# Optimization experiments

Hardware: AMD Instinct MI355X
Metric: run time of the kernel (lower is better)

Reference implementation:

```python
import jax, jax.numpy as jnp
import numpy as np

B, D, CTX, H = 262144, 16, 128, 192
IN_DIM = D + CTX + 1  # 145


def _linear_init(k, fan_in, fan_out):
    bound = 1.0 / np.sqrt(fan_in)
    kw, kb = jax.random.split(k)
    W = jax.random.uniform(kw, (fan_in, fan_out), jnp.float32, -bound, bound)
    b = jax.random.uniform(kb, (fan_out,), jnp.float32, -bound, bound)
    return W, b


def setup_inputs() -> dict:
    key = jax.random.key(0)
    ks = jax.random.split(key, 7)
    W1, b1 = _linear_init(ks[0], IN_DIM, H)
    W2, b2 = _linear_init(ks[1], H, H)
    W3, b3 = _linear_init(ks[2], H, D)
    return {
        "t": jax.random.uniform(ks[3], (), jnp.float32),
        "y": jax.random.normal(ks[4], (B, D), jnp.float32),
        "logp": jnp.zeros((B,), jnp.float32),
        "h": jax.random.normal(ks[5], (B, CTX), jnp.float32),
        "eps": jax.random.normal(ks[6], (B, D), jnp.float32),
        "W1": W1, "b1": b1, "W2": W2, "b2": b2, "W3": W3, "b3": b3,
    }


def _mlp(x, W1, b1, W2, b2, W3, b3):
    # 3-layer MLP, exact (erf) GELU as torch.nn.GELU default
    x = jax.nn.gelu(x @ W1 + b1, approximate=False)
    x = jax.nn.gelu(x @ W2 + b2, approximate=False)
    return x @ W3 + b3


def reference(t, y, logp, h, eps, W1, b1, W2, b2, W3, b3):
    Bsz = y.shape[0]
    t_feat = jnp.ones((Bsz, 1), y.dtype) * t

    def f_of_y(yy):
        inp = jnp.concatenate([yy, h, t_feat], axis=1)  # (B, D+CTX+1)
        return _mlp(inp, W1, b1, W2, b2, W3, b3)  # (B, D)

    # Hutchinson: torch computes g = J^T eps then (g*eps).sum(1) = eps^T J^T eps,
    # which per-row equals eps^T J eps = dot(eps, J eps). Forward-mode JVP computes
    # f and J eps in one fused pass (same math, no explicit backward graph).
    f, Jeps = jax.jvp(f_of_y, (y,), (eps,))
    trace = jnp.sum(Jeps * eps, axis=1)  # (B,)
    dlogp = -trace
    dh = jnp.zeros_like(h)
    return (f, dlogp, dh)
```

## Files before the change

kernel.cpp:

```cpp
#include <hip/hip_runtime.h>
#include <hip/hip_bf16.h>
#include <math.h>

#define B_TOTAL 262144
#define D 16
#define CTX 128
#define H 192
#define IN_DIM 145
#define KP1 160
#define M 32
#define BLOCK 256

typedef __attribute__((ext_vector_type(8))) short bf16x8;
typedef __attribute__((ext_vector_type(4))) float f32x4;

#define MFMA(a, b, c) __builtin_amdgcn_mfma_f32_16x16x32_bf16((a), (b), (c), 0, 0, 0)

__device__ __forceinline__ unsigned short f2bf_rne(float f) {
    unsigned u = __builtin_bit_cast(unsigned, f);
    u += 0x7FFFu + ((u >> 16) & 1u);
    return (unsigned short)(u >> 16);
}
__device__ __forceinline__ void split2(float v, unsigned short& hi, unsigned short& lo) {
    unsigned u = __builtin_bit_cast(unsigned, v);
    hi = (unsigned short)(u >> 16);
    float hf = __builtin_bit_cast(float, u & 0xFFFF0000u);
    lo = f2bf_rne(v - hf);
}
__device__ __forceinline__ void gelu_pair(float x, float& a, float& gp) {
    float s   = x * x;
    float e   = __expf(-0.5f * s);
    float az  = fabsf(x) * 0.70710678118654752f;
    float t   = __builtin_amdgcn_rcpf(fmaf(0.3275911f, az, 1.0f));
    float p   = t * (0.254829592f + t * (-0.284496736f + t * (1.421413741f +
                t * (-1.453152027f + t * 1.061405429f))));
    float erfv = __builtin_copysignf(1.0f - p * e, x);
    float phi  = fmaf(0.5f, erfv, 0.5f);
    gp = fmaf(0.39894228040143268f * x, e, phi);
    a  = x * phi;
}

__global__ void prep_weights(const float* __restrict__ W1,
                             const float* __restrict__ W2,
                             const float* __restrict__ W3,
                             unsigned short* __restrict__ wt)
{
    int i = blockIdx.x * 256 + threadIdx.x;
    if (i < H * KP1) {
        int n = i / KP1, kp = i % KP1;
        float v = 0.0f;
        if (kp < 16)       v = W1[kp * H + n];
        else if (kp == 16) v = W1[144 * H + n];
        else if (kp >= 32) v = W1[(kp - 16) * H + n];
        wt[i] = f2bf_rne(v);
        return;
    }
    i -= H * KP1;
    if (i < H * H) {
        int n = i / H, k = i % H;
        wt[30720 + i] = f2bf_rne(W2[k * H + n]);
        return;
    }
    i -= H * H;
    if (i < D * H) {
        int n = i / H, k = i % H;
        wt[67584 + i] = f2bf_rne(W3[k * D + n]);
    }
}

__global__ __launch_bounds__(BLOCK, 3) void odefunc_mfma(
    const float* __restrict__ t_ptr,
    const float* __restrict__ y,
    const float* __restrict__ h,
    const float* __restrict__ eps,
    const float* __restrict__ b1,
    const float* __restrict__ b2,
    const float* __restrict__ b3,
    const unsigned short* __restrict__ wt,
    float* __restrict__ out_f,
    float* __restrict__ out_dlogp,
    float* __restrict__ out_dh)
{
    __shared__ __align__(16) unsigned short Xh[M][168];
    __shared__ __align__(16) unsigned short Xl[M][40];
    __shared__ __align__(16) unsigned short Th[M][40], Tl[M][40];
    __shared__ __align__(16) unsigned short A[M][200], U[M][200];

    const int tid  = threadIdx.x;
    const int lane = tid & 63;
    const int wv   = tid >> 6;
    const int quad = lane >> 4;
    const int l16  = lane & 15;
    const size_t r0 = (size_t)blockIdx.x * M;

    const unsigned short* Wt1 = wt;
    const unsigned short* Wt2 = wt + 30720;
    const unsigned short* Wt3 = wt + 67584;

    {
        float4 z4 = {0.f, 0.f, 0.f, 0.f};
        #pragma unroll
        for (int i = 0; i < 4; ++i) {
            int idx = tid + i * BLOCK;
            int r = idx >> 5, c4 = (idx & 31) * 4;
            *(float4*)(out_dh + (r0 + r) * CTX + c4) = z4;
        }
    }

    {
        int task = tid >> 7, idx = tid & 127;
        int r = idx >> 2, d4 = (idx & 3) * 4;
        const float* src = task ? eps : y;
        float4 v = *(const float4*)(src + (r0 + r) * D + d4);
        ushort4 hi, lo;
        split2(v.x, hi.x, lo.x); split2(v.y, hi.y, lo.y);
        split2(v.z, hi.z, lo.z); split2(v.w, hi.w, lo.w);
        if (task == 0) { *(ushort4*)&Xh[r][d4] = hi; *(ushort4*)&Xl[r][d4] = lo; }
        else           { *(ushort4*)&Th[r][d4] = hi; *(ushort4*)&Tl[r][d4] = lo; }
    }
    if (tid < M) {
        int r = tid;
        float tv = t_ptr[0];
        unsigned short thi, tlo;
        split2(tv, thi, tlo);
        ushort4 z4 = {0, 0, 0, 0};
        ushort4 t4 = {thi, 0, 0, 0};
        ushort4 l4 = {tlo, 0, 0, 0};
        *(ushort4*)&Xh[r][16] = t4; *(ushort4*)&Xh[r][20] = z4;
        *(ushort4*)&Xh[r][24] = z4; *(ushort4*)&Xh[r][28] = z4;
        *(ushort4*)&Xl[r][16] = l4; *(ushort4*)&Xl[r][20] = z4;
        *(ushort4*)&Xl[r][24] = z4; *(ushort4*)&Xl[r][28] = z4;
        *(ushort4*)&Th[r][16] = z4; *(ushort4*)&Th[r][20] = z4;
        *(ushort4*)&Th[r][24] = z4; *(ushort4*)&Th[r][28] = z4;
        *(ushort4*)&Tl[r][16] = z4; *(ushort4*)&Tl[r][20] = z4;
        *(ushort4*)&Tl[r][24] = z4; *(ushort4*)&Tl[r][28] = z4;
    }
    #pragma unroll
    for (int i = 0; i < 4; ++i) {
        int idx = tid + i * BLOCK;
        int r = idx >> 5, c4 = (idx & 31) * 4;
        float4 v = *(const float4*)(h + (r0 + r) * CTX + c4);
        ushort4 hv = { f2bf_rne(v.x), f2bf_rne(v.y), f2bf_rne(v.z), f2bf_rne(v.w) };
        *(ushort4*)&Xh[r][32 + c4] = hv;
    }
    __syncthreads();

    const f32x4 zf = {0.f, 0.f, 0.f, 0.f};

    f32x4 z[2][3], u[2][3];
    #pragma unroll
    for (int rt = 0; rt < 2; ++rt)
        #pragma unroll
        for (int j = 0; j < 3; ++j) { z[rt][j] = zf; u[rt][j] = zf; }

    bf16x8 w1f[3][5];
    #pragma unroll
    for (int j = 0; j < 3; ++j) {
        int n = (wv * 3 + j) * 16 + l16;
        #pragma unroll
        for (int kc = 0; kc < 5; ++kc)
            w1f[j][kc] = *(const bf16x8*)(Wt1 + n * KP1 + kc * 32 + quad * 8);
    }
    #pragma unroll
    for (int kc = 0; kc < 5; ++kc)
        #pragma unroll
        for (int rt = 0; rt < 2; ++rt) {
            bf16x8 ah = *(const bf16x8*)&Xh[rt * 16 + l16][kc * 32 + quad * 8];
            #pragma unroll
            for (int j = 0; j < 3; ++j) z[rt][j] = MFMA(ah, w1f[j][kc], z[rt][j]);
        }
    #pragma unroll
    for (int rt = 0; rt < 2; ++rt) {
        int m = rt * 16 + l16;
        bf16x8 al = *(const bf16x8*)&Xl[m][quad * 8];
        bf16x8 th = *(const bf16x8*)&Th[m][quad * 8];
        bf16x8 tl = *(const bf16x8*)&Tl[m][quad * 8];
        #pragma unroll
        for (int j = 0; j < 3; ++j) {
            z[rt][j] = MFMA(al, w1f[j][0], z[rt][j]);
            u[rt][j] = MFMA(th, w1f[j][0], u[rt][j]);
            u[rt][j] = MFMA(tl, w1f[j][0], u[rt][j]);
        }
    }
    #pragma unroll
    for (int j = 0; j < 3; ++j) {
        int n = (wv * 3 + j) * 16 + l16;
        float bb = b1[n];
        #pragma unroll
        for (int rt = 0; rt < 2; ++rt)
            #pragma unroll
            for (int rg = 0; rg < 4; ++rg) {
                int m = rt * 16 + quad * 4 + rg;
                float x = z[rt][j][rg] + bb;
                float a, gp; gelu_pair(x, a, gp);
                A[m][n] = f2bf_rne(a);
                U[m][n] = f2bf_rne(u[rt][j][rg] * gp);
            }
    }
    __syncthreads();

    f32x4 z2[2][3], u2[2][3];
    #pragma unroll
    for (int rt = 0; rt < 2; ++rt)
        #pragma unroll
        for (int j = 0; j < 3; ++j) { z2[rt][j] = zf; u2[rt][j] = zf; }

    bf16x8 w2f[3][6];
    #pragma unroll
    for (int j = 0; j < 3; ++j) {
        int n = (wv * 3 + j) * 16 + l16;
        #pragma unroll
        for (int kc = 0; kc < 6; ++kc)
            w2f[j][kc] = *(const bf16x8*)(Wt2 + n * H + kc * 32 + quad * 8);
    }
    #pragma unroll
    for (int kc = 0; kc < 6; ++kc)
        #pragma unroll
        for (int rt = 0; rt < 2; ++rt) {
            int m = rt * 16 + l16, o = kc * 32 + quad * 8;
            bf16x8 av = *(const bf16x8*)&A[m][o];
            bf16x8 uv = *(const bf16x8*)&U[m][o];
            #pragma unroll
            for (int j = 0; j < 3; ++j) {
                z2[rt][j] = MFMA(av, w2f[j][kc], z2[rt][j]);
                u2[rt][j] = MFMA(uv, w2f[j][kc], u2[rt][j]);
            }
        }
    __syncthreads();
    #pragma unroll
    for (int j = 0; j < 3; ++j) {
        int n = (wv * 3 + j) * 16 + l16;
        float bb = b2[n];
        #pragma unroll
        for (int rt = 0; rt < 2; ++rt)
            #pragma unroll
            for (int rg = 0; rg < 4; ++rg) {
                int m = rt * 16 + quad * 4 + rg;
                float x = z2[rt][j][rg] + bb;
                float a, gp; gelu_pair(x, a, gp);
                A[m][n] = f2bf_rne(a);
                U[m][n] = f2bf_rne(u2[rt][j][rg] * gp);
            }
    }
    __syncthreads();

    {
        const int strm = wv & 1, rt = wv >> 1;
        const unsigned short (*P)[200] = strm ? U : A;

        bf16x8 w3f[6];
        #pragma unroll
        for (int kc = 0; kc < 6; ++kc)
            w3f[kc] = *(const bf16x8*)(Wt3 + l16 * H + kc * 32 + quad * 8);

        f32x4 acc = zf;
        #pragma unroll
        for (int kc = 0; kc < 6; ++kc) {
            bf16x8 xv = *(const bf16x8*)&P[rt * 16 + l16][kc * 32 + quad * 8];
            acc = MFMA(xv, w3f[kc], acc);
        }

        if (strm == 0) {
            float bb = b3[l16];
            #pragma unroll
            for (int rg = 0; rg < 4; ++rg) {
                int m = rt * 16 + quad * 4 + rg;
                out_f[(r0 + m) * D + l16] = acc[rg] + bb;
            }
        } else {
            float pr[4];
            #pragma unroll
            for (int rg = 0; rg < 4; ++rg) {
                int m = rt * 16 + quad * 4 + rg;
                pr[rg] = acc[rg] * eps[(r0 + m) * D + l16];
            }
            #pragma unroll
            for (int sh = 1; sh < 16; sh <<= 1)
                #pragma unroll
                for (int rg = 0; rg < 4; ++rg)
                    pr[rg] += __shfl_xor(pr[rg], sh, 64);
            if (l16 == 0)
                #pragma unroll
                for (int rg = 0; rg < 4; ++rg)
                    out_dlogp[r0 + rt * 16 + quad * 4 + rg] = -pr[rg];
        }
    }
}

extern "C" void kernel_launch(void* const* d_in, const int* in_sizes, int n_in,
                              void* d_out, int out_size, void* d_ws, size_t ws_size,
                              hipStream_t stream)
{
    const float* t   = (const float*)d_in[0];
    const float* y   = (const float*)d_in[1];
    const float* h   = (const float*)d_in[3];
    const float* eps = (const float*)d_in[4];
    const float* W1  = (const float*)d_in[5];
    const float* b1  = (const float*)d_in[6];
    const float* W2  = (const float*)d_in[7];
    const float* b2  = (const float*)d_in[8];
    const float* W3  = (const float*)d_in[9];
    const float* b3  = (const float*)d_in[10];

    float* out       = (float*)d_out;
    float* out_f     = out;
    float* out_dlogp = out + (size_t)B_TOTAL * D;
    float* out_dh    = out + (size_t)B_TOTAL * (D + 1);

    unsigned short* wt = (unsigned short*)d_ws;

    int prep_elems = H * KP1 + H * H + D * H;
    prep_weights<<<(prep_elems + 255) / 256, 256, 0, stream>>>(W1, W2, W3, wt);

    odefunc_mfma<<<B_TOTAL / M, BLOCK, 0, stream>>>(
        t, y, h, eps, b1, b2, b3, wt, out_f, out_dlogp, out_dh);
}
```

Measured before the change: 407.4 us.

## Alias LDS buffers, fold low-part K into padded W1, cheaper erf approx

Shared memory is repacked into one aliased byte buffer, so the layer-1 input tiles and the A activation buffer share space and the LDS footprint drops. The min-blocks launch bound is raised from 3 to 5 so more workgroups can be resident per CU. The y/t low-bf16 parts are moved into an extra K chunk of an extended W1 (K from 160 to 192), with a barrier added before A overwrites the aliased input. The erf polynomial is replaced with a shorter 3-term Abramowitz-Stegun form, which is cheaper but less accurate, and the higher occupancy target may force register spills.

```diff
diff --git a/kernel.cpp b/kernel.cpp
--- a/kernel.cpp
+++ b/kernel.cpp
@@ -6,8 +6,7 @@
 #define D 16
 #define CTX 128
 #define H 192
-#define IN_DIM 145
-#define KP1 160
+#define KX 192
 #define M 32
 #define BLOCK 256
 
@@ -28,13 +27,11 @@
     lo = f2bf_rne(v - hf);
 }
 __device__ __forceinline__ void gelu_pair(float x, float& a, float& gp) {
-    float s   = x * x;
-    float e   = __expf(-0.5f * s);
-    float az  = fabsf(x) * 0.70710678118654752f;
-    float t   = __builtin_amdgcn_rcpf(fmaf(0.3275911f, az, 1.0f));
-    float p   = t * (0.254829592f + t * (-0.284496736f + t * (1.421413741f +
-                t * (-1.453152027f + t * 1.061405429f))));
-    float erfv = __builtin_copysignf(1.0f - p * e, x);
+    float e    = __expf(-0.5f * x * x);
+    float az   = fabsf(x) * 0.70710678118654752f;
+    float t    = __builtin_amdgcn_rcpf(fmaf(0.47047f, az, 1.0f));
+    float p    = t * fmaf(t, fmaf(t, 0.7478556f, -0.0958798f), 0.3480242f);
+    float erfv = __builtin_copysignf(fmaf(-p, e, 1.0f), x);
     float phi  = fmaf(0.5f, erfv, 0.5f);
     gp = fmaf(0.39894228040143268f * x, e, phi);
     a  = x * phi;
@@ -46,29 +43,31 @@
                              unsigned short* __restrict__ wt)
 {
     int i = blockIdx.x * 256 + threadIdx.x;
-    if (i < H * KP1) {
-        int n = i / KP1, kp = i % KP1;
+    if (i < H * KX) {
+        int n = i / KX, kp = i % KX;
         float v = 0.0f;
-        if (kp < 16)       v = W1[kp * H + n];
-        else if (kp == 16) v = W1[144 * H + n];
-        else if (kp >= 32) v = W1[(kp - 16) * H + n];
+        if (kp < 16)                       v = W1[kp * H + n];
+        else if (kp == 16)                 v = W1[144 * H + n];
+        else if (kp >= 32 && kp < 160)     v = W1[(kp - 16) * H + n];
+        else if (kp >= 160 && kp < 176)    v = W1[(kp - 160) * H + n];
+        else if (kp == 176)                v = W1[144 * H + n];
         wt[i] = f2bf_rne(v);
         return;
     }
-    i -= H * KP1;
+    i -= H * KX;
     if (i < H * H) {
         int n = i / H, k = i % H;
-        wt[30720 + i] = f2bf_rne(W2[k * H + n]);
+        wt[36864 + i] = f2bf_rne(W2[k * H + n]);
         return;
     }
     i -= H * H;
     if (i < D * H) {
         int n = i / H, k = i % H;
-        wt[67584 + i] = f2bf_rne(W3[k * D + n]);
-    }
-}
-
-__global__ __launch_bounds__(BLOCK, 3) void odefunc_mfma(
+        wt[73728 + i] = f2bf_rne(W3[k * D + n]);
+    }
+}
+
+__global__ __launch_bounds__(BLOCK, 5) void odefunc_mfma(
     const float* __restrict__ t_ptr,
     const float* __restrict__ y,
     const float* __restrict__ h,
@@ -81,10 +80,11 @@
     float* __restrict__ out_dlogp,
     float* __restrict__ out_dh)
 {
-    __shared__ __align__(16) unsigned short Xh[M][168];
-    __shared__ __align__(16) unsigned short Xl[M][40];
-    __shared__ __align__(16) unsigned short Th[M][40], Tl[M][40];
-    __shared__ __align__(16) unsigned short A[M][200], U[M][200];
+    __shared__ __align__(16) unsigned char smem[30208];
+    unsigned short (*Xh)[200] = (unsigned short (*)[200])smem;
+    unsigned short (*Tc)[72]  = (unsigned short (*)[72])(smem + 12800);
+    unsigned short (*A)[200]  = (unsigned short (*)[200])smem;
+    unsigned short (*U)[200]  = (unsigned short (*)[200])(smem + 17408);
 
     const int tid  = threadIdx.x;
     const int lane = tid & 63;
@@ -94,8 +94,8 @@
     const size_t r0 = (size_t)blockIdx.x * M;
 
     const unsigned short* Wt1 = wt;
-    const unsigned short* Wt2 = wt + 30720;
-    const unsigned short* Wt3 = wt + 67584;
+    const unsigned short* Wt2 = wt + 36864;
+    const unsigned short* Wt3 = wt + 73728;
 
     {
         float4 z4 = {0.f, 0.f, 0.f, 0.f};
@@ -115,8 +115,8 @@
         ushort4 hi, lo;
         split2(v.x, hi.x, lo.x); split2(v.y, hi.y, lo.y);
         split2(v.z, hi.z, lo.z); split2(v.w, hi.w, lo.w);
-        if (task == 0) { *(ushort4*)&Xh[r][d4] = hi; *(ushort4*)&Xl[r][d4] = lo; }
-        else           { *(ushort4*)&Th[r][d4] = hi; *(ushort4*)&Tl[r][d4] = lo; }
+        if (task == 0) { *(ushort4*)&Xh[r][d4] = hi; *(ushort4*)&Xh[r][160 + d4] = lo; }
+        else           { *(ushort4*)&Tc[r][d4] = hi; *(ushort4*)&Tc[r][32 + d4] = lo; }
     }
     if (tid < M) {
         int r = tid;
@@ -126,14 +126,14 @@
         ushort4 z4 = {0, 0, 0, 0};
         ushort4 t4 = {thi, 0, 0, 0};
         ushort4 l4 = {tlo, 0, 0, 0};
-        *(ushort4*)&Xh[r][16] = t4; *(ushort4*)&Xh[r][20] = z4;
-        *(ushort4*)&Xh[r][24] = z4; *(ushort4*)&Xh[r][28] = z4;
-        *(ushort4*)&Xl[r][16] = l4; *(ushort4*)&Xl[r][20] = z4;
-        *(ushort4*)&Xl[r][24] = z4; *(ushort4*)&Xl[r][28] = z4;
-        *(ushort4*)&Th[r][16] = z4; *(ushort4*)&Th[r][20] = z4;
-        *(ushort4*)&Th[r][24] = z4; *(ushort4*)&Th[r][28] = z4;
-        *(ushort4*)&Tl[r][16] = z4; *(ushort4*)&Tl[r][20] = z4;
-        *(ushort4*)&Tl[r][24] = z4; *(ushort4*)&Tl[r][28] = z4;
+        *(ushort4*)&Xh[r][16]  = t4; *(ushort4*)&Xh[r][20]  = z4;
+        *(ushort4*)&Xh[r][24]  = z4; *(ushort4*)&Xh[r][28]  = z4;
+        *(ushort4*)&Xh[r][176] = l4; *(ushort4*)&Xh[r][180] = z4;
+        *(ushort4*)&Xh[r][184] = z4; *(ushort4*)&Xh[r][188] = z4;
+        *(ushort4*)&Tc[r][16]  = z4; *(ushort4*)&Tc[r][20]  = z4;
+        *(ushort4*)&Tc[r][24]  = z4; *(ushort4*)&Tc[r][28]  = z4;
+        *(ushort4*)&Tc[r][48]  = z4; *(ushort4*)&Tc[r][52]  = z4;
+        *(ushort4*)&Tc[r][56]  = z4; *(ushort4*)&Tc[r][60]  = z4;
     }
     #pragma unroll
     for (int i = 0; i < 4; ++i) {
@@ -153,16 +153,16 @@
         #pragma unroll
         for (int j = 0; j < 3; ++j) { z[rt][j] = zf; u[rt][j] = zf; }
 
-    bf16x8 w1f[3][5];
+    bf16x8 w1f[3][6];
     #pragma unroll
     for (int j = 0; j < 3; ++j) {
         int n = (wv * 3 + j) * 16 + l16;
         #pragma unroll
-        for (int kc = 0; kc < 5; ++kc)
-            w1f[j][kc] = *(const bf16x8*)(Wt1 + n * KP1 + kc * 32 + quad * 8);
-    }
-    #pragma unroll
-    for (int kc = 0; kc < 5; ++kc)
+        for (int kc = 0; kc < 6; ++kc)
+            w1f[j][kc] = *(const bf16x8*)(Wt1 + n * KX + kc * 32 + quad * 8);
+    }
+    #pragma unroll
+    for (int kc = 0; kc < 6; ++kc)
         #pragma unroll
         for (int rt = 0; rt < 2; ++rt) {
             bf16x8 ah = *(const bf16x8*)&Xh[rt * 16 + l16][kc * 32 + quad * 8];
@@ -172,16 +172,16 @@
     #pragma unroll
     for (int rt = 0; rt < 2; ++rt) {
         int m = rt * 16 + l16;
-        bf16x8 al = *(const bf16x8*)&Xl[m][quad * 8];
-        bf16x8 th = *(const bf16x8*)&Th[m][quad * 8];
-        bf16x8 tl = *(const bf16x8*)&Tl[m][quad * 8];
+        bf16x8 th = *(const bf16x8*)&Tc[m][quad * 8];
+        bf16x8 tl = *(const bf16x8*)&Tc[m][32 + quad * 8];
         #pragma unroll
         for (int j = 0; j < 3; ++j) {
-            z[rt][j] = MFMA(al, w1f[j][0], z[rt][j]);
             u[rt][j] = MFMA(th, w1f[j][0], u[rt][j]);
-            u[rt][j] = MFMA(tl, w1f[j][0], u[rt][j]);
-        }
-    }
+            u[rt][j] = MFMA(tl, w1f[j][5], u[rt][j]);
+        }
+    }
+    __syncthreads();
+
     #pragma unroll
     for (int j = 0; j < 3; ++j) {
         int n = (wv * 3 + j) * 16 + l16;
@@ -227,6 +227,7 @@
             }
         }
     __syncthreads();
+
     #pragma unroll
     for (int j = 0; j < 3; ++j) {
         int n = (wv * 3 + j) * 16 + l16;
@@ -309,7 +310,7 @@
 
     unsigned short* wt = (unsigned short*)d_ws;
 
-    int prep_elems = H * KP1 + H * H + D * H;
+    int prep_elems = H * KX + H * H + D * H;
     prep_weights<<<(prep_elems + 255) / 256, 256, 0, stream>>>(W1, W2, W3, wt);
 
     odefunc_mfma<<<B_TOTAL / M, BLOCK, 0, stream>>>(
```

Result: slower. 417.7 us (+2.5%).
